# Kernel tuning notes

Measured on AMD Instinct MI355X. Metric: run time of the kernel, lower is better.

Reference implementation:

```python
import jax, jax.numpy as jnp
import numpy as np

WINDOW = 2048
STEP = WINDOW // 2                 # 1024
N_SAMPLES = 131072
N_COEFFS = WINDOW // 2 + 1         # 1025
N_FRAMES = N_SAMPLES // STEP       # 128
Z_DIM = 128
BATCH, N_EVENTS, IMP_SAMPLES = 64, 1, 4096
BASE_RES = 0.02
RES_RANGE = (1.0 - BASE_RES) * 0.99


def setup_inputs() -> dict:
    key = jax.random.key(0)
    k1, k2, k3 = jax.random.split(key, 3)
    z = jax.random.normal(k1, (BATCH, N_EVENTS, Z_DIM), dtype=jnp.float32)
    impulse = jax.random.normal(k2, (BATCH, N_EVENTS, IMP_SAMPLES), dtype=jnp.float32)
    # stand-in for ConvUpsample: linear z -> (n_coeffs * n_frames)
    W_tf = jax.random.normal(k3, (Z_DIM, N_COEFFS * N_FRAMES), dtype=jnp.float32) * 0.02
    b_tf = jnp.zeros((N_COEFFS * N_FRAMES,), dtype=jnp.float32)
    return {"z": z, "impulse": impulse, "W_tf": W_tf, "b_tf": b_tf}


def _hann(n):
    # periodic hann (torch.hann_window default)
    return (0.5 - 0.5 * jnp.cos(2.0 * jnp.pi * jnp.arange(n) / n)).astype(jnp.float32)


def reference(z, impulse, W_tf, b_tf):
    B, E, imp_len = impulse.shape
    pad = N_SAMPLES - imp_len + WINDOW
    x = jnp.pad(impulse, ((0, 0), (0, 0), (0, pad)))  # (B,E,n_samples+window)
    win = _hann(WINDOW)

    # windowed_audio: overlapping frames * hann window -> (B,E,F,W)
    idx = jnp.arange(N_FRAMES)[:, None] * STEP + jnp.arange(WINDOW)[None, :]
    windowed = x[..., idx] * win

    # transfer functions: linear, reshape (C,F) -> transpose to (F,C), squash
    tf = (z.reshape(-1, Z_DIM) @ W_tf + b_tf).reshape(B, E, N_COEFFS, N_FRAMES)
    tf = jnp.transpose(tf, (0, 1, 3, 2))                       # (B,E,F,C)
    tf = BASE_RES + jax.nn.sigmoid(tf) * RES_RANGE

    cur_specs = jnp.fft.rfft(windowed, axis=-1)                # (B,E,F,C) complex64

    # advance_one_frame rotation: [re,im] @ [[c,-s],[s,-c]]
    g = jnp.linspace(0.0, np.pi, N_COEFFS).astype(jnp.float32)
    c, s = jnp.cos(g), jnp.sin(g)

    def step(prev_audio, inp):
        cur_spec, tfi = inp
        ps = jnp.fft.rfft(prev_audio, axis=-1)
        re, im = ps.real, ps.imag
        rot = jax.lax.complex(re * c + im * s, -(re * s + im * c))
        spec = (cur_spec + rot) * tfi
        audio = jnp.fft.irfft(spec, n=WINDOW, axis=-1)
        return audio, audio

    xs = (jnp.moveaxis(cur_specs, 2, 0), jnp.moveaxis(tf, 2, 0))
    init = jnp.zeros((B, E, WINDOW), dtype=jnp.float32)  # i==0: zero prev spec
    _, frames = jax.lax.scan(step, init, xs)             # (F,B,E,W)
    frames = jnp.moveaxis(frames, 0, 2) * win            # overlap_add apply_window=True

    # overlap-add with hop = WINDOW//2, vectorized via half-frame reshapes
    first = frames[..., :STEP].reshape(B, E, N_FRAMES * STEP)
    second = frames[..., STEP:].reshape(B, E, N_FRAMES * STEP)
    out = jnp.zeros((B, E, (N_FRAMES + 1) * STEP), dtype=jnp.float32)
    out = out.at[..., : N_FRAMES * STEP].add(first)
    out = out.at[..., STEP:].add(second)
    return out[..., :N_SAMPLES]
```

## Files before the change

### kernel.cpp

```cpp
#include <hip/hip_runtime.h>

#define NB 64
#define ZDIM 128
#define NCOEF 1025
#define NFR 128
#define COLS 131200
#define WINSZ 2048
#define HALFW 1024
#define NSAMP 131072
#define IMPN 4096
#define NCHUNK 32
#define NCK 31

#define TF_OFF   0
#define TF_SZ    (NB*COLS)
#define TFT_OFF  (TF_OFF + TF_SZ)
#define TFT_SZ   (NB*NFR*NCOEF)
#define CUR_OFF  (TFT_OFF + TFT_SZ)
#define CUR_SZ   (NB*4*NCOEF*2)
#define CK_OFF   (CUR_OFF + CUR_SZ)
#define CK_SZ    (NCK*NB*NCOEF*2)
#define WINT_OFF (CK_OFF + CK_SZ)
#define WINT_SZ  (WINSZ)
#define TW_OFF   (WINT_OFF + WINT_SZ)
#define TW_SZ    (HALFW*2)
#define ZBF_OFF  (TW_OFF + TW_SZ)
#define ZBF_SZ   (NB*ZDIM/2)

#define PHI(p) ((p) ^ ((((p) >> 4) & 3) << 2))

typedef short bf16x8 __attribute__((ext_vector_type(8)));
typedef float f32x4 __attribute__((ext_vector_type(4)));
typedef float f32x2 __attribute__((ext_vector_type(2)));

__device__ __forceinline__ f32x2 cmul2(f32x2 a, f32x2 b) {
  f32x2 t = f32x2{a.x, a.x} * b;
  return f32x2{-a.y, a.y} * f32x2{b.y, b.x} + t;
}
__device__ __forceinline__ f32x2 nid(f32x2 d) { return f32x2{d.y, -d.x}; }

#define WGBAR()                                              \
  do {                                                       \
    asm volatile("s_waitcnt lgkmcnt(0)" ::: "memory");       \
    __builtin_amdgcn_s_barrier();                            \
    asm volatile("" ::: "memory");                           \
  } while (0)

#define PIPEFENCE() asm volatile("" ::: "memory")

__device__ __forceinline__ short f2bf(float f) {
  unsigned u = __builtin_bit_cast(unsigned, f);
  u += 0x7FFFu + ((u >> 16) & 1u);
  return (short)(u >> 16);
}

__device__ __forceinline__ void gload_lds16(const float* g, float* l) {
  __builtin_amdgcn_global_load_lds(
      (const __attribute__((address_space(1))) unsigned int*)(const void*)g,
      (__attribute__((address_space(3))) unsigned int*)(void*)l, 16, 0, 0);
}

__global__ __launch_bounds__(256) void init_tables(const float* __restrict__ z,
                                                   float* __restrict__ winT,
                                                   float2* __restrict__ twG,
                                                   short* __restrict__ zbf) {
  int i = blockIdx.x * 256 + threadIdx.x;
  if (i < WINSZ) {
    winT[i] = 0.5f - 0.5f * cosf((float)(2.0 * 3.14159265358979323846 / 2048.0) * (float)i);
  }
  if (i < HALFW) {
    float ang = (float)(-2.0 * 3.14159265358979323846 / 2048.0) * (float)i;
    float sv, cv;
    sincosf(ang, &sv, &cv);
    twG[i] = make_float2(cv, sv);
  }
  if (i < NB * ZDIM) zbf[i] = f2bf(z[i]);
}

__global__ __launch_bounds__(256) void tf_gemm_mfma(const short* __restrict__ zbf,
                                                    const float* __restrict__ W,
                                                    const float* __restrict__ bias,
                                                    float* __restrict__ tf) {
  __shared__ float Wt[128 * 32];
  int tid = threadIdx.x;
  int wave = tid >> 6, lane = tid & 63;
  int colb = blockIdx.x * 32;

#pragma unroll
  for (int it = 0; it < 4; ++it) {
    int ci = tid + it * 256;
    const float* src = W + (size_t)(ci >> 3) * COLS + colb + (ci & 7) * 4;
    gload_lds16(src, &Wt[ci * 4]);
  }

  int lr = lane & 15;
  int lk = (lane >> 4) * 8;
  int lq = (lane >> 4) * 4;

  float bv[2];
#pragma unroll
  for (int n = 0; n < 2; ++n) bv[n] = bias[colb + 16 * n + lr];

  f32x4 acc[2];
#pragma unroll
  for (int n = 0; n < 2; ++n)
    acc[n] = f32x4{bv[n], bv[n], bv[n], bv[n]};

  bf16x8 afr[4];
#pragma unroll
  for (int s = 0; s < 4; ++s)
    afr[s] = *reinterpret_cast<const bf16x8*>(zbf + (16 * wave + lr) * ZDIM + s * 32 + lk);

  __syncthreads();

#pragma unroll
  for (int s = 0; s < 4; ++s) {
    bf16x8 bfr[2];
#pragma unroll
    for (int n = 0; n < 2; ++n) {
      const float* wp = &Wt[(s * 32 + lk) * 32 + 16 * n + lr];
      bfr[n] = bf16x8{f2bf(wp[0 * 32]), f2bf(wp[1 * 32]), f2bf(wp[2 * 32]), f2bf(wp[3 * 32]),
                      f2bf(wp[4 * 32]), f2bf(wp[5 * 32]), f2bf(wp[6 * 32]), f2bf(wp[7 * 32])};
    }
#pragma unroll
    for (int n = 0; n < 2; ++n)
      acc[n] = __builtin_amdgcn_mfma_f32_16x16x32_bf16(afr[s], bfr[n], acc[n], 0, 0, 0);
  }

  const float RESR = (1.0f - 0.02f) * 0.99f;
#pragma unroll
  for (int n = 0; n < 2; ++n) {
    int col = colb + 16 * n + lr;
#pragma unroll
    for (int r = 0; r < 4; ++r) {
      int row = 16 * wave + lq + r;
      float x = acc[n][r];
      float sg = 1.0f / (1.0f + __expf(-x));
      tf[(size_t)row * COLS + col] = 0.02f + sg * RESR;
    }
  }
}

static __device__ __forceinline__ void wg_fft2048(float* ar, float* ai,
                                                  float* br, float* bi,
                                                  const float2* tw,
                                                  float** outr, float** outi) {
  float *xr = ar, *xi = ai, *yr = br, *yi = bi;
  int m = 1;
  for (int s = 0; s < 11; ++s) {
    __syncthreads();
#pragma unroll
    for (int it = 0; it < 4; ++it) {
      int t = (int)threadIdx.x + it * 256;
      int jm = t & ~(m - 1);
      float x0r = xr[t], x0i = xi[t];
      float x1r = xr[t + 1024], x1i = xi[t + 1024];
      float2 w = tw[jm];
      float sr = x0r + x1r, si = x0i + x1i;
      float dr = x0r - x1r, di = x0i - x1i;
      float pr = dr * w.x - di * w.y;
      float pi = dr * w.y + di * w.x;
      yr[t + jm] = sr;      yi[t + jm] = si;
      yr[t + jm + m] = pr;  yi[t + jm + m] = pi;
    }
    float* t0 = xr; xr = yr; yr = t0;
    float* t1 = xi; xi = yi; yi = t1;
    m <<= 1;
  }
  __syncthreads();
  *outr = xr; *outi = xi;
}

__global__ __launch_bounds__(256) void fwd_fft_kernel(const float* __restrict__ imp,
                                                      const float* __restrict__ winT,
                                                      const float2* __restrict__ twG,
                                                      float2* __restrict__ cur) {
  __shared__ float b0r[WINSZ], b0i[WINSZ], b1r[WINSZ], b1i[WINSZ];
  __shared__ float2 tw[HALFW];
  int wg = blockIdx.x;
  int b = wg >> 2, f = wg & 3;
  int tid = threadIdx.x;

  for (int i = tid; i < HALFW; i += 256) tw[i] = twG[i];
  for (int w = tid; w < WINSZ; w += 256) {
    int s = f * HALFW + w;
    float v = (s < IMPN) ? imp[(size_t)b * IMPN + s] * winT[w] : 0.0f;
    b0r[w] = v;
    b0i[w] = 0.0f;
  }
  float *rr, *ri;
  wg_fft2048(b0r, b0i, b1r, b1i, tw, &rr, &ri);
  for (int k = tid; k < NCOEF; k += 256)
    cur[(size_t)wg * NCOEF + k] = make_float2(rr[k], ri[k]);
}

__global__ __launch_bounds__(256) void recur_ck_t(const float* __restrict__ tf,
                                                  const float2* __restrict__ cur,
                                                  float2* __restrict__ ckp,
                                                  float* __restrict__ tft) {
  int id = blockIdx.x * 256 + threadIdx.x;
  if (id >= NB * NCOEF) return;
  int b = id / NCOEF;
  int k = id - b * NCOEF;

  float g = 3.14159265358979323846f * (float)k / 1024.0f;
  float sg, cg;
  sincosf(g, &sg, &cg);
  bool herm = (k == 0) || (k == HALFW);

  const float4* tf4 = (const float4*)(tf + (size_t)b * COLS + (size_t)k * NFR);
  const float2* curb = cur + (size_t)b * 4 * NCOEF + k;
  float* tftb = tft + (size_t)b * NFR * NCOEF + k;

  float pre = 0.0f, pim = 0.0f;
  for (int f4 = 0; f4 < 32; ++f4) {
    float4 tv = tf4[f4];
    float tfs[4] = {tv.x, tv.y, tv.z, tv.w};
#pragma unroll
    for (int u = 0; u < 4; ++u) {
      int f = 4 * f4 + u;
      tftb[(size_t)f * NCOEF] = tfs[u];
      if (f < 124) {
        float tfv = tfs[u];
        float cr = 0.0f, ci = 0.0f;
        if (f < 4) {
          float2 cv = curb[(size_t)f * NCOEF];
          cr = cv.x; ci = cv.y;
        }
        float ire = herm ? 0.0f : pim;
        float rre = fmaf(pre, cg, ire * sg);
        float rim = -fmaf(pre, sg, ire * cg);
        float sre = (cr + rre) * tfv;
        float sim = (ci + rim) * tfv;
        if ((f & 3) == 2)
          ckp[(size_t)((f - 2) >> 2) * NB * NCOEF + (size_t)b * NCOEF + k] = make_float2(sre, sim);
        pre = sre; pim = sim;
      }
    }
  }
}

__global__ __launch_bounds__(256) void fused_resyn(const float* __restrict__ tft,
                                                   const float2* __restrict__ cur,
                                                   const float2* __restrict__ ckp,
                                                   const float* __restrict__ winT,
                                                   const float2* __restrict__ twG,
                                                   float* __restrict__ out) {
  __shared__ f32x2 P[1024];
  __shared__ f32x2 Q[1024];

  int bidx = blockIdx.x;
  int b = bidx >> 5, c = bidx & 31;
  int t = threadIdx.x;

  float pre[5], pim[5], cgv[5], sgv[5];
#pragma unroll
  for (int i = 0; i < 5; ++i) {
    if (i == 4) { cgv[4] = -1.0f; sgv[4] = 0.0f; }
    else {
      float2 tv = twG[t + 256 * i];
      cgv[i] = tv.x; sgv[i] = -tv.y;
    }
    pre[i] = 0.0f; pim[i] = 0.0f;
  }
  if (c > 0) {
    const float2* ck = ckp + ((size_t)(c - 1) * NB + b) * NCOEF;
#pragma unroll
    for (int i = 0; i < 5; ++i) {
      if (i == 4 && t != 0) continue;
      int k = (i == 4) ? 1024 : t + 256 * i;
      float2 v = ck[k];
      pre[i] = v.x; pim[i] = v.y;
    }
  }

  float2 tl;
  tl = twG[2 * t];          f32x2 w1a = f32x2{tl.x, tl.y};
  tl = twG[8 * (t & 63)];   f32x2 w2a = f32x2{tl.x, tl.y};
  tl = twG[32 * (t & 15)];  f32x2 w3a = f32x2{tl.x, tl.y};
  tl = twG[128 * (t & 3)];  f32x2 w4a = f32x2{tl.x, tl.y};
  tl = twG[t];              f32x2 twp0 = f32x2{tl.x, tl.y};

  const float Cs = 0.5f / 1024.0f;
  int mb = (t >> 6) + ((t >> 4) & 3) * 4 + ((t >> 2) & 3) * 16 + (t & 3) * 64;
  const float2* win2 = (const float2*)winT;
  f32x2 wv0, wv1, wv2, wv3;
  { float2 w = win2[mb];       wv0 = f32x2{w.x * Cs, w.y * Cs}; }
  { float2 w = win2[mb + 256]; wv1 = f32x2{w.x * Cs, w.y * Cs}; }
  { float2 w = win2[mb + 512]; wv2 = f32x2{w.x * Cs, w.y * Cs}; }
  { float2 w = win2[mb + 768]; wv3 = f32x2{w.x * Cs, w.y * Cs}; }

  int X0 = PHI(t);
  int B2 = 256 * (t >> 6) + ((t & 63) ^ (((t >> 4) & 3) << 2));
  int b3h = 64 * (t >> 4), i3 = t & 15;
  int b4h = 16 * (t >> 2), i4 = t & 3, c4 = (t >> 2) & 3;
  int p5 = b4h + 4 * ((t & 3) ^ c4);
  int pm0 = PHI((1024 - t) & 1023);
  int pm1 = PHI((1024 - (t + 256)) & 1023);
  int pm2 = PHI((1024 - (t + 512)) & 1023);
  int pm3 = PHI((1024 - (t + 768)) & 1023);

  const float* tftb = tft + (size_t)b * NFR * NCOEF;
  const float2* curb = cur + (size_t)b * 4 * NCOEF;

  int fs = (c == 0) ? 0 : 4 * c - 1;
  int fe = 4 * c + 3;
  f32x2 car0 = f32x2{0.0f, 0.0f}, car1 = f32x2{0.0f, 0.0f};

  float ntf[5];
  {
    const float* tfr = tftb + (size_t)fs * NCOEF;
#pragma unroll
    for (int i = 0; i < 4; ++i) ntf[i] = tfr[t + 256 * i];
    ntf[4] = (t == 0) ? tfr[1024] : 0.0f;
  }

#define KEEP(x) asm volatile("" : "+v"(x))

  for (int f = fs; f <= fe; ++f) {
    KEEP(w1a); KEEP(w2a); KEEP(w3a); KEEP(w4a); KEEP(twp0);

    float ctf[5];
#pragma unroll
    for (int i = 0; i < 5; ++i) ctf[i] = ntf[i];

    if (f < fe) {
      const float* tfr = tftb + (size_t)(f + 1) * NCOEF;
#pragma unroll
      for (int i = 0; i < 4; ++i) ntf[i] = tfr[t + 256 * i];
      ntf[4] = (t == 0) ? tfr[1024] : 0.0f;
    }

    float S[5], I[5];
#pragma unroll
    for (int i = 0; i < 5; ++i) {
      if (i == 4 && t != 0) { S[4] = 0.0f; I[4] = 0.0f; continue; }
      float cr = 0.0f, ci = 0.0f;
      if (f < 4) {
        int k = (i == 4) ? 1024 : t + 256 * i;
        float2 cv = curb[(size_t)f * NCOEF + k];
        cr = cv.x; ci = cv.y;
      }
      float rre = fmaf(pre[i], cgv[i], pim[i] * sgv[i]);
      float rim = -fmaf(pre[i], sgv[i], pim[i] * cgv[i]);
      S[i] = (cr + rre) * ctf[i];
      I[i] = (ci + rim) * ctf[i];
      pre[i] = S[i]; pim[i] = I[i];
    }

#pragma unroll
    for (int i = 0; i < 4; ++i)
      P[X0 + 256 * i] = f32x2{S[i], I[i]};
    WGBAR();

    const float R2 = 0.70710678118654752f;
    f32x2 twp1 = cmul2(twp0, f32x2{R2, -R2});
    f32x2 twp2 = f32x2{twp0.y, -twp0.x};
    f32x2 twp3 = f32x2{twp1.y, -twp1.x};
    f32x2 Z[4];
    {
      f32x2 xm[4];
      xm[0] = (t == 0) ? f32x2{S[4], 0.0f} : P[pm0];
      xm[1] = P[pm1]; xm[2] = P[pm2]; xm[3] = P[pm3];
      f32x2 twp[4] = {twp0, twp1, twp2, twp3};
#pragma unroll
      for (int i = 0; i < 4; ++i) {
        f32x2 x = f32x2{S[i], I[i]};
        f32x2 cjm = f32x2{xm[i].x, -xm[i].y};
        f32x2 xe = x + cjm;
        f32x2 xp = x - cjm;
        f32x2 Xo = cmul2(xp, f32x2{twp[i].x, -twp[i].y});
        Z[i] = f32x2{xe.x - Xo.y, -(xe.y + Xo.x)};
      }
    }
    {
      f32x2 w1b = cmul2(w1a, w1a);
      f32x2 w1c = cmul2(w1b, w1a);
      f32x2 A = Z[0] + Z[2];
      f32x2 B = Z[0] - Z[2];
      f32x2 C = Z[1] + Z[3];
      f32x2 D = Z[1] - Z[3];
      f32x2 nD = nid(D);
      Q[X0]       = A + C;
      Q[X0 + 256] = cmul2(B + nD, w1a);
      Q[X0 + 512] = cmul2(A - C, w1b);
      Q[X0 + 768] = cmul2(B - nD, w1c);
    }
    WGBAR();

    {
      f32x2 u0 = Q[B2], u1 = Q[B2 + 64], u2 = Q[B2 + 128], u3 = Q[B2 + 192];
      f32x2 w2b = cmul2(w2a, w2a);
      f32x2 w2c = cmul2(w2b, w2a);
      f32x2 A = u0 + u2, B = u0 - u2, C = u1 + u3, D = u1 - u3;
      f32x2 nD = nid(D);
      Q[B2]       = A + C;
      Q[B2 + 64]  = cmul2(B + nD, w2a);
      Q[B2 + 128] = cmul2(A - C, w2b);
      Q[B2 + 192] = cmul2(B - nD, w2c);
    }
    PIPEFENCE();

    {
      f32x2 u0 = Q[b3h + i3];
      f32x2 u1 = Q[b3h + 16 + (i3 ^ 4)];
      f32x2 u2 = Q[b3h + 32 + (i3 ^ 8)];
      f32x2 u3 = Q[b3h + 48 + (i3 ^ 12)];
      f32x2 w3b = cmul2(w3a, w3a);
      f32x2 w3c = cmul2(w3b, w3a);
      f32x2 A = u0 + u2, B = u0 - u2, C = u1 + u3, D = u1 - u3;
      f32x2 nD = nid(D);
      Q[b3h + i3]             = A + C;
      Q[b3h + 16 + (i3 ^ 4)]  = cmul2(B + nD, w3a);
      Q[b3h + 32 + (i3 ^ 8)]  = cmul2(A - C, w3b);
      Q[b3h + 48 + (i3 ^ 12)] = cmul2(B - nD, w3c);
    }
    PIPEFENCE();

    {
      f32x2 u0 = Q[b4h + 4 * (0 ^ c4) + i4];
      f32x2 u1 = Q[b4h + 4 * (1 ^ c4) + i4];
      f32x2 u2 = Q[b4h + 4 * (2 ^ c4) + i4];
      f32x2 u3 = Q[b4h + 4 * (3 ^ c4) + i4];
      f32x2 w4b = cmul2(w4a, w4a);
      f32x2 w4c = cmul2(w4b, w4a);
      f32x2 A = u0 + u2, B = u0 - u2, C = u1 + u3, D = u1 - u3;
      f32x2 nD = nid(D);
      Q[b4h + 4 * (0 ^ c4) + i4] = A + C;
      Q[b4h + 4 * (1 ^ c4) + i4] = cmul2(B + nD, w4a);
      Q[b4h + 4 * (2 ^ c4) + i4] = cmul2(A - C, w4b);
      Q[b4h + 4 * (3 ^ c4) + i4] = cmul2(B - nD, w4c);
    }
    PIPEFENCE();

    float4 q01 = *reinterpret_cast<const float4*>(&Q[p5]);
    float4 q23 = *reinterpret_cast<const float4*>(&Q[p5 + 2]);
    f32x2 z0, z1, z2, z3;
    {
      f32x2 a = f32x2{q01.x, q01.y}, bq = f32x2{q01.z, q01.w};
      f32x2 cq = f32x2{q23.x, q23.y}, d = f32x2{q23.z, q23.w};
      f32x2 A = a + cq, B = a - cq, C = bq + d, D = bq - d;
      f32x2 nD = nid(D);
      z0 = A + C;
      z1 = B + nD;
      z2 = A - C;
      z3 = B - nD;
    }

    f32x2 e0 = f32x2{z0.x, -z0.y} * wv0;
    f32x2 e1 = f32x2{z1.x, -z1.y} * wv1;
    f32x2 e2 = f32x2{z2.x, -z2.y} * wv2;
    f32x2 e3 = f32x2{z3.x, -z3.y} * wv3;
    if (f >= 4 * c) {
      f32x2* ob2 = (f32x2*)(out + (size_t)b * NSAMP + (size_t)f * 1024);
      ob2[mb]       = e0 + car0;
      ob2[mb + 256] = e1 + car1;
    }
    car0 = e2;
    car1 = e3;
  }
#undef KEEP
}

extern "C" void kernel_launch(void* const* d_in, const int* in_sizes, int n_in,
                              void* d_out, int out_size, void* d_ws, size_t ws_size,
                              hipStream_t stream) {
  const float* z    = (const float*)d_in[0];
  const float* imp  = (const float*)d_in[1];
  const float* W    = (const float*)d_in[2];
  const float* bias = (const float*)d_in[3];

  float* ws = (float*)d_ws;
  float*  tf   = ws + TF_OFF;
  float*  tft  = ws + TFT_OFF;
  float2* cur  = (float2*)(ws + CUR_OFF);
  float2* ckp  = (float2*)(ws + CK_OFF);
  float*  winT = ws + WINT_OFF;
  float2* twG  = (float2*)(ws + TW_OFF);
  short*  zbf  = (short*)(ws + ZBF_OFF);
  float*  out  = (float*)d_out;

  init_tables<<<32, 256, 0, stream>>>(z, winT, twG, zbf);
  tf_gemm_mfma<<<COLS / 32, 256, 0, stream>>>(zbf, W, bias, tf);
  fwd_fft_kernel<<<NB * 4, 256, 0, stream>>>(imp, winT, twG, cur);
  recur_ck_t<<<(NB * NCOEF + 255) / 256, 256, 0, stream>>>(tf, cur, ckp, tft);
  fused_resyn<<<NB * NCHUNK, 256, 0, stream>>>(tft, cur, ckp, winT, twG, out);
}
```

Baseline: 85.43 us.

## Halve frame chunks and process two frames per iteration in fused resynthesis

Reduces the number of frame chunks from 32 to 16, so each block handles 8 frames instead of 4, and the checkpoint kernel stores spectra every 8 frames. The resynthesis loop now runs two independent inverse FFTs per iteration using doubled shared buffers, which halves the number of barriers per frame and gives more instruction-level parallelism. The cost is half as many blocks (1024 instead of 2048), more shared memory and registers per block, and a longer serial chain of frames per block.

```diff
diff --git a/kernel.cpp b/kernel.cpp
--- a/kernel.cpp
+++ b/kernel.cpp
@@ -9,8 +9,8 @@
 #define HALFW 1024
 #define NSAMP 131072
 #define IMPN 4096
-#define NCHUNK 32
-#define NCK 31
+#define NCHUNK 16
+#define NCK 15
 
 #define TF_OFF   0
 #define TF_SZ    (NB*COLS)
@@ -220,7 +220,7 @@
     for (int u = 0; u < 4; ++u) {
       int f = 4 * f4 + u;
       tftb[(size_t)f * NCOEF] = tfs[u];
-      if (f < 124) {
+      if (f < 120) {
         float tfv = tfs[u];
         float cr = 0.0f, ci = 0.0f;
         if (f < 4) {
@@ -232,8 +232,8 @@
         float rim = -fmaf(pre, sg, ire * cg);
         float sre = (cr + rre) * tfv;
         float sim = (ci + rim) * tfv;
-        if ((f & 3) == 2)
-          ckp[(size_t)((f - 2) >> 2) * NB * NCOEF + (size_t)b * NCOEF + k] = make_float2(sre, sim);
+        if ((f & 7) == 6)
+          ckp[(size_t)((f - 6) >> 3) * NB * NCOEF + (size_t)b * NCOEF + k] = make_float2(sre, sim);
         pre = sre; pim = sim;
       }
     }
@@ -246,11 +246,11 @@
                                                    const float* __restrict__ winT,
                                                    const float2* __restrict__ twG,
                                                    float* __restrict__ out) {
-  __shared__ f32x2 P[1024];
-  __shared__ f32x2 Q[1024];
+  __shared__ f32x2 PA[1024], QA[1024];
+  __shared__ f32x2 PB[1024], QB[1024];
 
   int bidx = blockIdx.x;
-  int b = bidx >> 5, c = bidx & 31;
+  int b = bidx >> 4, c = bidx & 15;
   int t = threadIdx.x;
 
   float pre[5], pim[5], cgv[5], sgv[5];
@@ -303,38 +303,48 @@
   const float* tftb = tft + (size_t)b * NFR * NCOEF;
   const float2* curb = cur + (size_t)b * 4 * NCOEF;
 
-  int fs = (c == 0) ? 0 : 4 * c - 1;
-  int fe = 4 * c + 3;
+  int fs = (c == 0) ? 0 : 8 * c - 1;
+  int fe = 8 * c + 7;
+  int f0 = 8 * c;
   f32x2 car0 = f32x2{0.0f, 0.0f}, car1 = f32x2{0.0f, 0.0f};
 
-  float ntf[5];
+  float ntfA[5], ntfB[5];
   {
-    const float* tfr = tftb + (size_t)fs * NCOEF;
-#pragma unroll
-    for (int i = 0; i < 4; ++i) ntf[i] = tfr[t + 256 * i];
-    ntf[4] = (t == 0) ? tfr[1024] : 0.0f;
+    const float* ta = tftb + (size_t)fs * NCOEF;
+    const float* tb = tftb + (size_t)(fs + 1) * NCOEF;
+#pragma unroll
+    for (int i = 0; i < 4; ++i) { ntfA[i] = ta[t + 256 * i]; ntfB[i] = tb[t + 256 * i]; }
+    ntfA[4] = (t == 0) ? ta[1024] : 0.0f;
+    ntfB[4] = (t == 0) ? tb[1024] : 0.0f;
   }
 
 #define KEEP(x) asm volatile("" : "+v"(x))
 
-  for (int f = fs; f <= fe; ++f) {
+  for (int f = fs; f <= fe; f += 2) {
+    bool hasB = (f + 1 <= fe);
     KEEP(w1a); KEEP(w2a); KEEP(w3a); KEEP(w4a); KEEP(twp0);
 
-    float ctf[5];
-#pragma unroll
-    for (int i = 0; i < 5; ++i) ctf[i] = ntf[i];
-
-    if (f < fe) {
-      const float* tfr = tftb + (size_t)(f + 1) * NCOEF;
-#pragma unroll
-      for (int i = 0; i < 4; ++i) ntf[i] = tfr[t + 256 * i];
-      ntf[4] = (t == 0) ? tfr[1024] : 0.0f;
-    }
-
-    float S[5], I[5];
+    float ctfA[5], ctfB[5];
+#pragma unroll
+    for (int i = 0; i < 5; ++i) { ctfA[i] = ntfA[i]; ctfB[i] = ntfB[i]; }
+
+    if (f + 2 <= fe) {
+      const float* ta = tftb + (size_t)(f + 2) * NCOEF;
+#pragma unroll
+      for (int i = 0; i < 4; ++i) ntfA[i] = ta[t + 256 * i];
+      ntfA[4] = (t == 0) ? ta[1024] : 0.0f;
+      if (f + 3 <= fe) {
+        const float* tb = tftb + (size_t)(f + 3) * NCOEF;
+#pragma unroll
+        for (int i = 0; i < 4; ++i) ntfB[i] = tb[t + 256 * i];
+        ntfB[4] = (t == 0) ? tb[1024] : 0.0f;
+      }
+    }
+
+    float sA[5], iA[5], sB[5], iB[5];
 #pragma unroll
     for (int i = 0; i < 5; ++i) {
-      if (i == 4 && t != 0) { S[4] = 0.0f; I[4] = 0.0f; continue; }
+      if (i == 4 && t != 0) { sA[4] = 0.0f; iA[4] = 0.0f; continue; }
       float cr = 0.0f, ci = 0.0f;
       if (f < 4) {
         int k = (i == 4) ? 1024 : t + 256 * i;
@@ -343,121 +353,210 @@
       }
       float rre = fmaf(pre[i], cgv[i], pim[i] * sgv[i]);
       float rim = -fmaf(pre[i], sgv[i], pim[i] * cgv[i]);
-      S[i] = (cr + rre) * ctf[i];
-      I[i] = (ci + rim) * ctf[i];
-      pre[i] = S[i]; pim[i] = I[i];
-    }
-
-#pragma unroll
-    for (int i = 0; i < 4; ++i)
-      P[X0 + 256 * i] = f32x2{S[i], I[i]};
+      sA[i] = (cr + rre) * ctfA[i];
+      iA[i] = (ci + rim) * ctfA[i];
+      pre[i] = sA[i]; pim[i] = iA[i];
+    }
+    if (hasB) {
+#pragma unroll
+      for (int i = 0; i < 5; ++i) {
+        if (i == 4 && t != 0) { sB[4] = 0.0f; iB[4] = 0.0f; continue; }
+        float cr = 0.0f, ci = 0.0f;
+        if (f + 1 < 4) {
+          int k = (i == 4) ? 1024 : t + 256 * i;
+          float2 cv = curb[(size_t)(f + 1) * NCOEF + k];
+          cr = cv.x; ci = cv.y;
+        }
+        float rre = fmaf(pre[i], cgv[i], pim[i] * sgv[i]);
+        float rim = -fmaf(pre[i], sgv[i], pim[i] * cgv[i]);
+        sB[i] = (cr + rre) * ctfB[i];
+        iB[i] = (ci + rim) * ctfB[i];
+        pre[i] = sB[i]; pim[i] = iB[i];
+      }
+    } else {
+#pragma unroll
+      for (int i = 0; i < 5; ++i) { sB[i] = 0.0f; iB[i] = 0.0f; }
+    }
+
+#pragma unroll
+    for (int i = 0; i < 4; ++i) {
+      PA[X0 + 256 * i] = f32x2{sA[i], iA[i]};
+      PB[X0 + 256 * i] = f32x2{sB[i], iB[i]};
+    }
     WGBAR();
 
     const float R2 = 0.70710678118654752f;
     f32x2 twp1 = cmul2(twp0, f32x2{R2, -R2});
     f32x2 twp2 = f32x2{twp0.y, -twp0.x};
     f32x2 twp3 = f32x2{twp1.y, -twp1.x};
-    f32x2 Z[4];
-    {
-      f32x2 xm[4];
-      xm[0] = (t == 0) ? f32x2{S[4], 0.0f} : P[pm0];
-      xm[1] = P[pm1]; xm[2] = P[pm2]; xm[3] = P[pm3];
+    f32x2 w1b = cmul2(w1a, w1a);
+    f32x2 w1c = cmul2(w1b, w1a);
+    {
       f32x2 twp[4] = {twp0, twp1, twp2, twp3};
+      f32x2 ZA[4], ZB[4];
 #pragma unroll
       for (int i = 0; i < 4; ++i) {
-        f32x2 x = f32x2{S[i], I[i]};
-        f32x2 cjm = f32x2{xm[i].x, -xm[i].y};
-        f32x2 xe = x + cjm;
-        f32x2 xp = x - cjm;
-        f32x2 Xo = cmul2(xp, f32x2{twp[i].x, -twp[i].y});
-        Z[i] = f32x2{xe.x - Xo.y, -(xe.y + Xo.x)};
-      }
-    }
-    {
-      f32x2 w1b = cmul2(w1a, w1a);
-      f32x2 w1c = cmul2(w1b, w1a);
-      f32x2 A = Z[0] + Z[2];
-      f32x2 B = Z[0] - Z[2];
-      f32x2 C = Z[1] + Z[3];
-      f32x2 D = Z[1] - Z[3];
-      f32x2 nD = nid(D);
-      Q[X0]       = A + C;
-      Q[X0 + 256] = cmul2(B + nD, w1a);
-      Q[X0 + 512] = cmul2(A - C, w1b);
-      Q[X0 + 768] = cmul2(B - nD, w1c);
+        int pm = (i == 0) ? pm0 : (i == 1) ? pm1 : (i == 2) ? pm2 : pm3;
+        f32x2 tw_c = f32x2{twp[i].x, -twp[i].y};
+        {
+          f32x2 x = f32x2{sA[i], iA[i]};
+          f32x2 xm = (i == 0 && t == 0) ? f32x2{sA[4], 0.0f} : PA[pm];
+          f32x2 cjm = f32x2{xm.x, -xm.y};
+          f32x2 xe = x + cjm;
+          f32x2 xp = x - cjm;
+          f32x2 Xo = cmul2(xp, tw_c);
+          ZA[i] = f32x2{xe.x - Xo.y, -(xe.y + Xo.x)};
+        }
+        {
+          f32x2 x = f32x2{sB[i], iB[i]};
+          f32x2 xm = (i == 0 && t == 0) ? f32x2{sB[4], 0.0f} : PB[pm];
+          f32x2 cjm = f32x2{xm.x, -xm.y};
+          f32x2 xe = x + cjm;
+          f32x2 xp = x - cjm;
+          f32x2 Xo = cmul2(xp, tw_c);
+          ZB[i] = f32x2{xe.x - Xo.y, -(xe.y + Xo.x)};
+        }
+      }
+      {
+        f32x2 A = ZA[0] + ZA[2], B = ZA[0] - ZA[2];
+        f32x2 C = ZA[1] + ZA[3], D = ZA[1] - ZA[3];
+        f32x2 nD = nid(D);
+        QA[X0]       = A + C;
+        QA[X0 + 256] = cmul2(B + nD, w1a);
+        QA[X0 + 512] = cmul2(A - C, w1b);
+        QA[X0 + 768] = cmul2(B - nD, w1c);
+      }
+      {
+        f32x2 A = ZB[0] + ZB[2], B = ZB[0] - ZB[2];
+        f32x2 C = ZB[1] + ZB[3], D = ZB[1] - ZB[3];
+        f32x2 nD = nid(D);
+        QB[X0]       = A + C;
+        QB[X0 + 256] = cmul2(B + nD, w1a);
+        QB[X0 + 512] = cmul2(A - C, w1b);
+        QB[X0 + 768] = cmul2(B - nD, w1c);
+      }
     }
     WGBAR();
 
     {
-      f32x2 u0 = Q[B2], u1 = Q[B2 + 64], u2 = Q[B2 + 128], u3 = Q[B2 + 192];
       f32x2 w2b = cmul2(w2a, w2a);
       f32x2 w2c = cmul2(w2b, w2a);
-      f32x2 A = u0 + u2, B = u0 - u2, C = u1 + u3, D = u1 - u3;
-      f32x2 nD = nid(D);
-      Q[B2]       = A + C;
-      Q[B2 + 64]  = cmul2(B + nD, w2a);
-      Q[B2 + 128] = cmul2(A - C, w2b);
-      Q[B2 + 192] = cmul2(B - nD, w2c);
+      f32x2 a0 = QA[B2], a1 = QA[B2 + 64], a2 = QA[B2 + 128], a3 = QA[B2 + 192];
+      f32x2 b0 = QB[B2], b1 = QB[B2 + 64], b2 = QB[B2 + 128], b3 = QB[B2 + 192];
+      {
+        f32x2 A = a0 + a2, B = a0 - a2, C = a1 + a3, D = a1 - a3;
+        f32x2 nD = nid(D);
+        QA[B2]       = A + C;
+        QA[B2 + 64]  = cmul2(B + nD, w2a);
+        QA[B2 + 128] = cmul2(A - C, w2b);
+        QA[B2 + 192] = cmul2(B - nD, w2c);
+      }
+      {
+        f32x2 A = b0 + b2, B = b0 - b2, C = b1 + b3, D = b1 - b3;
+        f32x2 nD = nid(D);
+        QB[B2]       = A + C;
+        QB[B2 + 64]  = cmul2(B + nD, w2a);
+        QB[B2 + 128] = cmul2(A - C, w2b);
+        QB[B2 + 192] = cmul2(B - nD, w2c);
+      }
     }
     PIPEFENCE();
 
     {
-      f32x2 u0 = Q[b3h + i3];
-      f32x2 u1 = Q[b3h + 16 + (i3 ^ 4)];
-      f32x2 u2 = Q[b3h + 32 + (i3 ^ 8)];
-      f32x2 u3 = Q[b3h + 48 + (i3 ^ 12)];
       f32x2 w3b = cmul2(w3a, w3a);
       f32x2 w3c = cmul2(w3b, w3a);
-      f32x2 A = u0 + u2, B = u0 - u2, C = u1 + u3, D = u1 - u3;
-      f32x2 nD = nid(D);
-      Q[b3h + i3]             = A + C;
-      Q[b3h + 16 + (i3 ^ 4)]  = cmul2(B + nD, w3a);
-      Q[b3h + 32 + (i3 ^ 8)]  = cmul2(A - C, w3b);
-      Q[b3h + 48 + (i3 ^ 12)] = cmul2(B - nD, w3c);
+      int q0 = b3h + i3, q1 = b3h + 16 + (i3 ^ 4), q2 = b3h + 32 + (i3 ^ 8), q3 = b3h + 48 + (i3 ^ 12);
+      f32x2 a0 = QA[q0], a1 = QA[q1], a2 = QA[q2], a3 = QA[q3];
+      f32x2 b0 = QB[q0], b1 = QB[q1], b2 = QB[q2], b3 = QB[q3];
+      {
+        f32x2 A = a0 + a2, B = a0 - a2, C = a1 + a3, D = a1 - a3;
+        f32x2 nD = nid(D);
+        QA[q0] = A + C;
+        QA[q1] = cmul2(B + nD, w3a);
+        QA[q2] = cmul2(A - C, w3b);
+        QA[q3] = cmul2(B - nD, w3c);
+      }
+      {
+        f32x2 A = b0 + b2, B = b0 - b2, C = b1 + b3, D = b1 - b3;
+        f32x2 nD = nid(D);
+        QB[q0] = A + C;
+        QB[q1] = cmul2(B + nD, w3a);
+        QB[q2] = cmul2(A - C, w3b);
+        QB[q3] = cmul2(B - nD, w3c);
+      }
     }
     PIPEFENCE();
 
     {
-      f32x2 u0 = Q[b4h + 4 * (0 ^ c4) + i4];
-      f32x2 u1 = Q[b4h + 4 * (1 ^ c4) + i4];
-      f32x2 u2 = Q[b4h + 4 * (2 ^ c4) + i4];
-      f32x2 u3 = Q[b4h + 4 * (3 ^ c4) + i4];
       f32x2 w4b = cmul2(w4a, w4a);
       f32x2 w4c = cmul2(w4b, w4a);
-      f32x2 A = u0 + u2, B = u0 - u2, C = u1 + u3, D = u1 - u3;
-      f32x2 nD = nid(D);
-      Q[b4h + 4 * (0 ^ c4) + i4] = A + C;
-      Q[b4h + 4 * (1 ^ c4) + i4] = cmul2(B + nD, w4a);
-      Q[b4h + 4 * (2 ^ c4) + i4] = cmul2(A - C, w4b);
-      Q[b4h + 4 * (3 ^ c4) + i4] = cmul2(B - nD, w4c);
+      int q0 = b4h + 4 * (0 ^ c4) + i4, q1 = b4h + 4 * (1 ^ c4) + i4;
+      int q2 = b4h + 4 * (2 ^ c4) + i4, q3 = b4h + 4 * (3 ^ c4) + i4;
+      f32x2 a0 = QA[q0], a1 = QA[q1], a2 = QA[q2], a3 = QA[q3];
+      f32x2 b0 = QB[q0], b1 = QB[q1], b2 = QB[q2], b3 = QB[q3];
+      {
+        f32x2 A = a0 + a2, B = a0 - a2, C = a1 + a3, D = a1 - a3;
+        f32x2 nD = nid(D);
+        QA[q0] = A + C;
+        QA[q1] = cmul2(B + nD, w4a);
+        QA[q2] = cmul2(A - C, w4b);
+        QA[q3] = cmul2(B - nD, w4c);
+      }
+      {
+        f32x2 A = b0 + b2, B = b0 - b2, C = b1 + b3, D = b1 - b3;
+        f32x2 nD = nid(D);
+        QB[q0] = A + C;
+        QB[q1] = cmul2(B + nD, w4a);
+        QB[q2] = cmul2(A - C, w4b);
+        QB[q3] = cmul2(B - nD, w4c);
+      }
     }
     PIPEFENCE();
 
-    float4 q01 = *reinterpret_cast<const float4*>(&Q[p5]);
-    float4 q23 = *reinterpret_cast<const float4*>(&Q[p5 + 2]);
-    f32x2 z0, z1, z2, z3;
-    {
-      f32x2 a = f32x2{q01.x, q01.y}, bq = f32x2{q01.z, q01.w};
-      f32x2 cq = f32x2{q23.x, q23.y}, d = f32x2{q23.z, q23.w};
+    float4 qa01 = *reinterpret_cast<const float4*>(&QA[p5]);
+    float4 qa23 = *reinterpret_cast<const float4*>(&QA[p5 + 2]);
+    float4 qb01 = *reinterpret_cast<const float4*>(&QB[p5]);
+    float4 qb23 = *reinterpret_cast<const float4*>(&QB[p5 + 2]);
+    f32x2 zA0, zA1, zA2, zA3, zB0, zB1, zB2, zB3;
+    {
+      f32x2 a = f32x2{qa01.x, qa01.y}, bq = f32x2{qa01.z, qa01.w};
+      f32x2 cq = f32x2{qa23.x, qa23.y}, d = f32x2{qa23.z, qa23.w};
       f32x2 A = a + cq, B = a - cq, C = bq + d, D = bq - d;
       f32x2 nD = nid(D);
-      z0 = A + C;
-      z1 = B + nD;
-      z2 = A - C;
-      z3 = B - nD;
-    }
-
-    f32x2 e0 = f32x2{z0.x, -z0.y} * wv0;
-    f32x2 e1 = f32x2{z1.x, -z1.y} * wv1;
-    f32x2 e2 = f32x2{z2.x, -z2.y} * wv2;
-    f32x2 e3 = f32x2{z3.x, -z3.y} * wv3;
-    if (f >= 4 * c) {
-      f32x2* ob2 = (f32x2*)(out + (size_t)b * NSAMP + (size_t)f * 1024);
+      zA0 = A + C; zA1 = B + nD; zA2 = A - C; zA3 = B - nD;
+    }
+    {
+      f32x2 a = f32x2{qb01.x, qb01.y}, bq = f32x2{qb01.z, qb01.w};
+      f32x2 cq = f32x2{qb23.x, qb23.y}, d = f32x2{qb23.z, qb23.w};
+      f32x2 A = a + cq, B = a - cq, C = bq + d, D = bq - d;
+      f32x2 nD = nid(D);
+      zB0 = A + C; zB1 = B + nD; zB2 = A - C; zB3 = B - nD;
+    }
+
+    {
+      f32x2 e0 = f32x2{zA0.x, -zA0.y} * wv0;
+      f32x2 e1 = f32x2{zA1.x, -zA1.y} * wv1;
+      f32x2 e2 = f32x2{zA2.x, -zA2.y} * wv2;
+      f32x2 e3 = f32x2{zA3.x, -zA3.y} * wv3;
+      if (f >= f0) {
+        f32x2* ob2 = (f32x2*)(out + (size_t)b * NSAMP + (size_t)f * 1024);
+        ob2[mb]       = e0 + car0;
+        ob2[mb + 256] = e1 + car1;
+      }
+      car0 = e2;
+      car1 = e3;
+    }
+    if (hasB) {
+      f32x2 e0 = f32x2{zB0.x, -zB0.y} * wv0;
+      f32x2 e1 = f32x2{zB1.x, -zB1.y} * wv1;
+      f32x2 e2 = f32x2{zB2.x, -zB2.y} * wv2;
+      f32x2 e3 = f32x2{zB3.x, -zB3.y} * wv3;
+      f32x2* ob2 = (f32x2*)(out + (size_t)b * NSAMP + (size_t)(f + 1) * 1024);
       ob2[mb]       = e0 + car0;
       ob2[mb + 256] = e1 + car1;
-    }
-    car0 = e2;
-    car1 = e3;
+      car0 = e2;
+      car1 = e3;
+    }
   }
 #undef KEEP
 }
```

New measurement: 87.14 us. +2.0%, slower.
